# Performance work log

Measured on AMD Instinct MI355X. Metric: run time of the kernel, lower is better.

The kernel has to match this reference:

```python
import jax, jax.numpy as jnp
import numpy as np

NUM_EMBEDDINGS = 1024
EMBEDDING_DIM = 256
COMMITMENT_COST = 0.25
STRAIGHT_THROUGH = True


def setup_inputs() -> dict:
    key = jax.random.key(0)
    k_in, k_emb = jax.random.split(key)
    inputs = jax.random.normal(k_in, (32, 32, 32, EMBEDDING_DIM), dtype=jnp.float32)
    # variance_scaling(1.0, 'fan_in', 'uniform') over (K, D): limit = sqrt(3 / fan_in)
    limit = np.sqrt(3.0 / EMBEDDING_DIM).astype(np.float32)
    embedding = jax.random.uniform(
        k_emb, (NUM_EMBEDDINGS, EMBEDDING_DIM), dtype=jnp.float32,
        minval=-limit, maxval=limit)
    return {"inputs": inputs, "embedding": embedding}


def reference(inputs, embedding):
    input_shape = inputs.shape
    flat = jnp.reshape(inputs, (-1, EMBEDDING_DIM))  # [N, D]
    # squared euclidean distances [N, K]
    distances = (jnp.sum(flat ** 2, axis=1, keepdims=True)
                 - 2.0 * jnp.matmul(flat, embedding.T)
                 + jnp.sum(embedding ** 2, axis=1)[None, :])
    encoding_indices = jnp.argmin(distances, axis=1)  # [N]
    quantized = jnp.take(embedding, encoding_indices, axis=0)  # [N, D] gather == one-hot matmul
    quantized = jnp.reshape(quantized, input_shape)
    if STRAIGHT_THROUGH:
        quantized = inputs + jax.lax.stop_gradient(quantized - inputs)
    else:
        quantized = jax.lax.stop_gradient(quantized)
    e_latent_loss = jnp.mean((jax.lax.stop_gradient(quantized) - inputs) ** 2)
    q_latent_loss = jnp.mean((quantized - jax.lax.stop_gradient(inputs)) ** 2)
    vq_loss = q_latent_loss + COMMITMENT_COST * e_latent_loss
    return quantized, vq_loss, encoding_indices
```

## Files before the change

### kernel.cpp

```cpp
#include <hip/hip_runtime.h>

#define NPTS 32768
#define DIM 256
#define KCODES 1024
#define NSPLIT 8
#define BN 256
#define BKC 128
#define BK 64
#define MARGIN 0.08f

typedef __attribute__((ext_vector_type(8))) short short8v;
typedef __attribute__((ext_vector_type(8))) unsigned short ushort8v;
typedef __attribute__((ext_vector_type(4))) float f32x4;

static __device__ __forceinline__ unsigned short f2bf(float f) {
    unsigned int u = __float_as_uint(f);
    unsigned int r = (u + 0x7fffu + ((u >> 16) & 1u)) >> 16;
    return (unsigned short)r;
}

static __device__ __forceinline__ void gload16(const void* g, void* l) {
    __builtin_amdgcn_global_load_lds((const __attribute__((address_space(1))) void*)g,
                                     (__attribute__((address_space(3))) void*)l, 16, 0, 0);
}

__global__ void convert_kernel(const float* __restrict__ X, const float* __restrict__ E,
                               unsigned short* __restrict__ Xb, unsigned short* __restrict__ Eb) {
    int i = blockIdx.x * 256 + threadIdx.x;
    size_t e8 = (size_t)i * 8;
    const float* src; unsigned short* dst; size_t off;
    if (e8 < (size_t)NPTS * DIM) { src = X; dst = Xb; off = e8; }
    else { src = E; dst = Eb; off = e8 - (size_t)NPTS * DIM; }
    float4 f0 = *(const float4*)(src + off);
    float4 f1 = *(const float4*)(src + off + 4);
    ushort8v v;
    v[0] = f2bf(f0.x); v[1] = f2bf(f0.y); v[2] = f2bf(f0.z); v[3] = f2bf(f0.w);
    v[4] = f2bf(f1.x); v[5] = f2bf(f1.y); v[6] = f2bf(f1.z); v[7] = f2bf(f1.w);
    *(ushort8v*)(dst + off) = v;
}

__global__ void enormnp_kernel(const float* __restrict__ E, float* __restrict__ Cnp,
                               int* __restrict__ counter) {
#pragma clang fp contract(off)
    if (blockIdx.x == 0 && threadIdx.x == 0) counter[0] = 0;
    int k = blockIdx.x * 256 + threadIdx.x;
    const float* e = E + (size_t)k * DIM;
    float half[2];
    for (int h = 0; h < 2; ++h) {
        const float* b = e + h * 128;
        float s[8];
#pragma unroll
        for (int j = 0; j < 8; ++j) { float v = b[j]; s[j] = v * v; }
        for (int i = 8; i < 128; i += 8) {
#pragma unroll
            for (int j = 0; j < 8; ++j) { float v = b[i + j]; s[j] += v * v; }
        }
        half[h] = ((s[0] + s[1]) + (s[2] + s[3])) + ((s[4] + s[5]) + (s[6] + s[7]));
    }
    Cnp[k] = half[0] + half[1];
}

__global__ __launch_bounds__(256, 2) void dist_kernel(
        const unsigned short* __restrict__ Xb, const unsigned short* __restrict__ Eb,
        const float* __restrict__ Cnp,
        float* __restrict__ ws_mm, unsigned int* __restrict__ cand) {
    __shared__ unsigned short xs[BN * BK];
    __shared__ unsigned short es[BKC * BK];

    const int tid = threadIdx.x;
    const int lane = tid & 63;
    const int wave = tid >> 6;
    const int lg = lane >> 4, lc = lane & 15;
    const int pbase = blockIdx.x * BN;
    const int split = blockIdx.y;
    const int cbase = split * BKC;

    f32x4 acc[4][8];
#pragma unroll
    for (int i = 0; i < 4; ++i)
#pragma unroll
        for (int j = 0; j < 8; ++j) acc[i][j] = (f32x4){0.f, 0.f, 0.f, 0.f};

    for (int ks = 0; ks < DIM / BK; ++ks) {
        const int k0 = ks * BK;
        __syncthreads();
#pragma unroll
        for (int q = 0; q < 8; ++q) {
            const int B = wave * 8192 + q * 1024 + lane * 16;
            const int row = B >> 7;
            const int cs = ((B >> 4) & 7) ^ (row & 7);
            gload16(Xb + (size_t)(pbase + row) * DIM + k0 + cs * 8,
                    (char*)xs + wave * 8192 + q * 1024);
        }
#pragma unroll
        for (int q = 0; q < 4; ++q) {
            const int B = wave * 4096 + q * 1024 + lane * 16;
            const int row = B >> 7;
            const int cs = ((B >> 4) & 7) ^ (row & 7);
            gload16(Eb + (size_t)(cbase + row) * DIM + k0 + cs * 8,
                    (char*)es + wave * 4096 + q * 1024);
        }
        __syncthreads();
#pragma unroll
        for (int kk = 0; kk < 2; ++kk) {
            short8v a[4];
#pragma unroll
            for (int f = 0; f < 4; ++f) {
                int row = wave * 64 + f * 16 + lc;
                int cs = (kk * 4 + lg) ^ (row & 7);
                a[f] = *(const short8v*)&xs[row * BK + cs * 8];
            }
#pragma unroll
            for (int j = 0; j < 8; ++j) {
                int row = j * 16 + lc;
                int cs = (kk * 4 + lg) ^ (row & 7);
                short8v b = *(const short8v*)&es[row * BK + cs * 8];
#pragma unroll
                for (int i = 0; i < 4; ++i)
                    acc[i][j] = __builtin_amdgcn_mfma_f32_16x16x32_bf16(a[i], b, acc[i][j], 0, 0, 0);
            }
        }
    }

    float en8[8];
#pragma unroll
    for (int j = 0; j < 8; ++j) en8[j] = Cnp[cbase + j * 16 + lc];

    float m1[4][4], m2[4][4];
#pragma unroll
    for (int i = 0; i < 4; ++i)
#pragma unroll
        for (int r = 0; r < 4; ++r) { m1[i][r] = 3.4e38f; m2[i][r] = 3.4e38f; }

#pragma unroll
    for (int j = 0; j < 8; ++j)
#pragma unroll
        for (int i = 0; i < 4; ++i)
#pragma unroll
            for (int r = 0; r < 4; ++r) {
                float d = __builtin_fmaf(-2.f, acc[i][j][r], en8[j]);
                m2[i][r] = fminf(fmaxf(d, m1[i][r]), m2[i][r]);
                m1[i][r] = fminf(d, m1[i][r]);
            }

#pragma unroll
    for (int m = 1; m < 16; m <<= 1) {
#pragma unroll
        for (int i = 0; i < 4; ++i)
#pragma unroll
            for (int r = 0; r < 4; ++r) {
                float o1 = __shfl_xor(m1[i][r], m);
                float o2 = __shfl_xor(m2[i][r], m);
                float mx = fmaxf(m1[i][r], o1);
                m1[i][r] = fminf(m1[i][r], o1);
                m2[i][r] = fminf(fminf(m2[i][r], o2), mx);
            }
    }

#pragma unroll
    for (int i = 0; i < 4; ++i)
#pragma unroll
        for (int r = 0; r < 4; ++r) {
            float thr = m1[i][r] + MARGIN;
            unsigned int sl[8];
#pragma unroll
            for (int j = 0; j < 8; ++j) {
                float d = __builtin_fmaf(-2.f, acc[i][j][r], en8[j]);
                unsigned long long mm = __ballot(d <= thr);
                sl[j] = (unsigned int)((mm >> (lg * 16)) & 0xFFFFull);
            }
            if (lc == 0) {
                int p = pbase + wave * 64 + i * 16 + lg * 4 + r;
                uint4 w4 = { sl[0] | (sl[1] << 16), sl[2] | (sl[3] << 16),
                             sl[4] | (sl[5] << 16), sl[6] | (sl[7] << 16) };
                *(uint4*)&cand[((size_t)p * NSPLIT + split) * 4] = w4;
                float2 mm2 = { m1[i][r], m2[i][r] };
                *(float2*)&ws_mm[((size_t)p * NSPLIT + split) * 2] = mm2;
            }
        }
}

__global__ void resolve_kernel(const float* __restrict__ ws_mm, const unsigned int* __restrict__ cand,
                               int* __restrict__ final_idx, int* __restrict__ list,
                               int* __restrict__ counter) {
    const int p = blockIdx.x * 256 + threadIdx.x;
    float v1 = 3.4e38f, v2 = 3.4e38f;
    int sstar = 0;
#pragma unroll
    for (int s = 0; s < NSPLIT; ++s) {
        float2 mm = *(const float2*)&ws_mm[((size_t)p * NSPLIT + s) * 2];
        if (mm.x < v1) {
            v2 = fminf(v1, mm.y); v1 = mm.x; sstar = s;
        } else {
            v2 = fminf(v2, mm.x);
        }
    }
    uint4 w4 = *(const uint4*)&cand[((size_t)p * NSPLIT + sstar) * 4];
    int idx;
    if (w4.x)      idx = __builtin_ctz(w4.x);
    else if (w4.y) idx = 32 + __builtin_ctz(w4.y);
    else if (w4.z) idx = 64 + __builtin_ctz(w4.z);
    else           idx = 96 + __builtin_ctz(w4.w);
    final_idx[p] = sstar * BKC + idx;

    float thr = v1 + MARGIN;
    if (v2 <= thr) {
        int slot = atomicAdd(counter, 1);
        list[slot] = p;
    }
}

__global__ __launch_bounds__(256) void rescore_np_kernel(
        const float* __restrict__ X, const float* __restrict__ E,
        const float* __restrict__ Cnp, const unsigned int* __restrict__ cand,
        const int* __restrict__ list, const int* __restrict__ counter,
        int* __restrict__ final_idx) {
#pragma clang fp contract(off)
    const int tid = threadIdx.x;
    const int lane = tid & 63;
    const int wave = tid >> 6;
    const int cnt = counter[0];
    __shared__ float xsh[4][DIM];

    for (int base = blockIdx.x * 4; base < cnt; base += gridDim.x * 4) {
        const int li = base + wave;
        const bool active = (li < cnt);
        const int p = list[active ? li : (cnt - 1)];
        __syncthreads();
        *(float4*)&xsh[wave][lane * 4] = *(const float4*)(X + (size_t)p * DIM + lane * 4);
        __syncthreads();

        float s = 0.f;
        if (lane < 16) {
            const int h = lane >> 3, j = lane & 7;
            float v = xsh[wave][h * 128 + j];
            s = v * v;
            for (int i = 8; i < 128; i += 8) {
                float w = xsh[wave][h * 128 + i + j];
                s += w * w;
            }
        }
        float t0 = __shfl(s, 0), t1 = __shfl(s, 1), t2 = __shfl(s, 2), t3 = __shfl(s, 3);
        float t4 = __shfl(s, 4), t5 = __shfl(s, 5), t6 = __shfl(s, 6), t7 = __shfl(s, 7);
        float u0 = __shfl(s, 8), u1 = __shfl(s, 9), u2 = __shfl(s, 10), u3 = __shfl(s, 11);
        float u4 = __shfl(s, 12), u5 = __shfl(s, 13), u6 = __shfl(s, 14), u7 = __shfl(s, 15);
        const float A = (((t0 + t1) + (t2 + t3)) + ((t4 + t5) + (t6 + t7)))
                      + (((u0 + u1) + (u2 + u3)) + ((u4 + u5) + (u6 + u7)));

        float bv = 3.4e38f; int bi = 0x7FFFFFFF;
        if (lane < 32) {
            unsigned int bits = cand[(size_t)p * 32 + lane];
            const int cb = (lane >> 2) * 128 + (lane & 3) * 32;
            while (bits) {
                int t = __builtin_ctz(bits);
                bits &= bits - 1;
                int c = cb + t;
                const float4* er4 = (const float4*)(E + (size_t)c * DIM);
                float acc = 0.f;
                for (int d4 = 0; d4 < DIM / 4; ++d4) {
                    float4 e4 = er4[d4];
                    float4 x4 = *(const float4*)&xsh[wave][d4 * 4];
                    acc = __builtin_fmaf(x4.x, e4.x, acc);
                    acc = __builtin_fmaf(x4.y, e4.y, acc);
                    acc = __builtin_fmaf(x4.z, e4.z, acc);
                    acc = __builtin_fmaf(x4.w, e4.w, acc);
                }
                float tt = A - 2.0f * acc;
                float dnp = tt + Cnp[c];
                if (dnp < bv) { bv = dnp; bi = c; }
            }
        }
#pragma unroll
        for (int m = 1; m < 64; m <<= 1) {
            float ov = __shfl_xor(bv, m);
            int oi = __shfl_xor(bi, m);
            if (ov < bv || (ov == bv && oi < bi)) { bv = ov; bi = oi; }
        }
        if (active && lane == 0) final_idx[p] = bi;
    }
}

__global__ void gather_kernel(const float* __restrict__ X, const float* __restrict__ E,
                              const int* __restrict__ final_idx,
                              float* __restrict__ out_q, float* __restrict__ out_idx,
                              float* __restrict__ ws_part) {
    const int tid = threadIdx.x;
    const int p = blockIdx.x * 16 + (tid >> 4);
    const int c = tid & 15;
    const int bi = final_idx[p];

    float ls = 0.f;
#pragma unroll
    for (int k = 0; k < 4; ++k) {
        int d4 = c + k * 16;
        float4 e4 = *(const float4*)(E + (size_t)bi * DIM + d4 * 4);
        float4 x4 = *(const float4*)(X + (size_t)p * DIM + d4 * 4);
        *(float4*)(out_q + (size_t)p * DIM + d4 * 4) = e4;
        float dx = e4.x - x4.x, dy = e4.y - x4.y, dz = e4.z - x4.z, dw = e4.w - x4.w;
        ls += dx * dx + dy * dy + dz * dz + dw * dw;
    }
    if (c == 0) out_idx[p] = (float)bi;

    __shared__ float red[256];
    red[tid] = ls;
    __syncthreads();
#pragma unroll
    for (int s = 128; s > 0; s >>= 1) {
        if (tid < s) red[tid] += red[tid + s];
        __syncthreads();
    }
    if (tid == 0) ws_part[blockIdx.x] = red[0];
}

__global__ void loss_kernel(const float* __restrict__ ws_part, float* __restrict__ out_loss) {
    const int tid = threadIdx.x;
    float s = 0.f;
    for (int i = tid; i < NPTS / 16; i += 256) s += ws_part[i];
    __shared__ float red[256];
    red[tid] = s;
    __syncthreads();
#pragma unroll
    for (int t = 128; t > 0; t >>= 1) {
        if (tid < t) red[tid] += red[tid + t];
        __syncthreads();
    }
    if (tid == 0)
        out_loss[0] = (1.f + 0.25f) * red[0] / (float)((size_t)NPTS * DIM);
}

extern "C" void kernel_launch(void* const* d_in, const int* in_sizes, int n_in,
                              void* d_out, int out_size, void* d_ws, size_t ws_size,
                              hipStream_t stream) {
    const float* X = (const float*)d_in[0];
    const float* E = (const float*)d_in[1];
    float* out = (float*)d_out;
    float* out_q = out;
    float* out_loss = out + (size_t)NPTS * DIM;
    float* out_idx = out + (size_t)NPTS * DIM + 1;

    unsigned short* Xb = (unsigned short*)d_out;
    unsigned short* Eb = Xb + (size_t)NPTS * DIM;
    unsigned int* cand = (unsigned int*)(Eb + (size_t)KCODES * DIM);

    float* ws = (float*)d_ws;
    float* Cnp = ws;
    float* ws_mm = Cnp + KCODES;
    int* final_idx = (int*)(ws_mm + (size_t)NPTS * NSPLIT * 2);
    int* counter = final_idx + NPTS;
    int* list = counter + 64;
    float* ws_part = (float*)(list + NPTS);

    convert_kernel<<<(NPTS + KCODES) * DIM / 8 / 256, 256, 0, stream>>>(X, E, Xb, Eb);
    enormnp_kernel<<<KCODES / 256, 256, 0, stream>>>(E, Cnp, counter);
    dist_kernel<<<dim3(NPTS / BN, NSPLIT), 256, 0, stream>>>(Xb, Eb, Cnp, ws_mm, cand);
    resolve_kernel<<<NPTS / 256, 256, 0, stream>>>(ws_mm, cand, final_idx, list, counter);
    rescore_np_kernel<<<512, 256, 0, stream>>>(X, E, Cnp, cand, list, counter, final_idx);
    gather_kernel<<<NPTS / 16, 256, 0, stream>>>(X, E, final_idx, out_q, out_idx, ws_part);
    loss_kernel<<<1, 256, 0, stream>>>(ws_part, out_loss);
}
```

Measured before the change: 98.20 us.

## Fuse codebook norms into convert, compute loss from distances, drop second-min tracking

Folds the codebook-norm computation into the conversion kernel as extra blocks, and accumulates per-point ||x||^2 during conversion. The loss is then assembled from ||x||^2 plus the best bf16-approximate distance inside resolve via a last-block reduction, so gather no longer rereads X and the separate loss kernel is removed. Dist_kernel keeps only the running minimum, no second minimum, and raises launch bounds to 3 blocks per CU. Ambiguity is detected from the per-split minima and candidate popcount. Risks: the loss now uses approximate (bf16) distances that are not rescored, and register pressure rises under the tighter occupancy target.

```diff
diff --git a/kernel.cpp b/kernel.cpp
--- a/kernel.cpp
+++ b/kernel.cpp
@@ -8,6 +8,7 @@
 #define BKC 128
 #define BK 64
 #define MARGIN 0.08f
+#define CVT_BLOCKS 2048
 
 typedef __attribute__((ext_vector_type(8))) short short8v;
 typedef __attribute__((ext_vector_type(8))) unsigned short ushort8v;
@@ -25,45 +26,62 @@
 }
 
 __global__ void convert_kernel(const float* __restrict__ X, const float* __restrict__ E,
-                               unsigned short* __restrict__ Xb, unsigned short* __restrict__ Eb) {
-    int i = blockIdx.x * 256 + threadIdx.x;
-    size_t e8 = (size_t)i * 8;
-    const float* src; unsigned short* dst; size_t off;
-    if (e8 < (size_t)NPTS * DIM) { src = X; dst = Xb; off = e8; }
-    else { src = E; dst = Eb; off = e8 - (size_t)NPTS * DIM; }
-    float4 f0 = *(const float4*)(src + off);
-    float4 f1 = *(const float4*)(src + off + 4);
-    ushort8v v;
-    v[0] = f2bf(f0.x); v[1] = f2bf(f0.y); v[2] = f2bf(f0.z); v[3] = f2bf(f0.w);
-    v[4] = f2bf(f1.x); v[5] = f2bf(f1.y); v[6] = f2bf(f1.z); v[7] = f2bf(f1.w);
-    *(ushort8v*)(dst + off) = v;
-}
-
-__global__ void enormnp_kernel(const float* __restrict__ E, float* __restrict__ Cnp,
-                               int* __restrict__ counter) {
+                               unsigned short* __restrict__ Xb, unsigned short* __restrict__ Eb,
+                               float* __restrict__ Cnp, float* __restrict__ xsq_part) {
 #pragma clang fp contract(off)
-    if (blockIdx.x == 0 && threadIdx.x == 0) counter[0] = 0;
-    int k = blockIdx.x * 256 + threadIdx.x;
-    const float* e = E + (size_t)k * DIM;
-    float half[2];
-    for (int h = 0; h < 2; ++h) {
-        const float* b = e + h * 128;
-        float s[8];
-#pragma unroll
-        for (int j = 0; j < 8; ++j) { float v = b[j]; s[j] = v * v; }
-        for (int i = 8; i < 128; i += 8) {
-#pragma unroll
-            for (int j = 0; j < 8; ++j) { float v = b[i + j]; s[j] += v * v; }
-        }
-        half[h] = ((s[0] + s[1]) + (s[2] + s[3])) + ((s[4] + s[5]) + (s[6] + s[7]));
-    }
-    Cnp[k] = half[0] + half[1];
-}
-
-__global__ __launch_bounds__(256, 2) void dist_kernel(
+    const int tid = threadIdx.x;
+    if (blockIdx.x >= CVT_BLOCKS) {
+        int k = (blockIdx.x - CVT_BLOCKS) * 256 + tid;
+        const float* e = E + (size_t)k * DIM;
+        float half[2];
+        for (int h = 0; h < 2; ++h) {
+            const float* b = e + h * 128;
+            float s[8];
+#pragma unroll
+            for (int j = 0; j < 8; ++j) { float v = b[j]; s[j] = v * v; }
+            for (int i = 8; i < 128; i += 8) {
+#pragma unroll
+                for (int j = 0; j < 8; ++j) { float v = b[i + j]; s[j] += v * v; }
+            }
+            half[h] = ((s[0] + s[1]) + (s[2] + s[3])) + ((s[4] + s[5]) + (s[6] + s[7]));
+        }
+        Cnp[k] = half[0] + half[1];
+        return;
+    }
+    const int total = (NPTS + KCODES) * DIM / 8;
+    float xsq = 0.f;
+    for (int i = blockIdx.x * 256 + tid; i < total; i += CVT_BLOCKS * 256) {
+        size_t e8 = (size_t)i * 8;
+        const float* src; unsigned short* dst; size_t off;
+        bool isX = e8 < (size_t)NPTS * DIM;
+        if (isX) { src = X; dst = Xb; off = e8; }
+        else { src = E; dst = Eb; off = e8 - (size_t)NPTS * DIM; }
+        float4 f0 = *(const float4*)(src + off);
+        float4 f1 = *(const float4*)(src + off + 4);
+        ushort8v v;
+        v[0] = f2bf(f0.x); v[1] = f2bf(f0.y); v[2] = f2bf(f0.z); v[3] = f2bf(f0.w);
+        v[4] = f2bf(f1.x); v[5] = f2bf(f1.y); v[6] = f2bf(f1.z); v[7] = f2bf(f1.w);
+        *(ushort8v*)(dst + off) = v;
+        if (isX)
+            xsq += f0.x * f0.x + f0.y * f0.y + f0.z * f0.z + f0.w * f0.w
+                 + f1.x * f1.x + f1.y * f1.y + f1.z * f1.z + f1.w * f1.w;
+    }
+    __shared__ float red[256];
+    red[tid] = xsq;
+    __syncthreads();
+#pragma unroll
+    for (int s = 128; s > 0; s >>= 1) {
+        if (tid < s) red[tid] += red[tid + s];
+        __syncthreads();
+    }
+    if (tid == 0) xsq_part[blockIdx.x] = red[0];
+}
+
+__global__ __launch_bounds__(256, 3) void dist_kernel(
         const unsigned short* __restrict__ Xb, const unsigned short* __restrict__ Eb,
         const float* __restrict__ Cnp,
-        float* __restrict__ ws_mm, unsigned int* __restrict__ cand) {
+        float* __restrict__ ws_m1, unsigned int* __restrict__ cand,
+        int* __restrict__ counters) {
     __shared__ unsigned short xs[BN * BK];
     __shared__ unsigned short es[BKC * BK];
 
@@ -75,6 +93,8 @@
     const int split = blockIdx.y;
     const int cbase = split * BKC;
 
+    if (blockIdx.x == 0 && split == 0 && tid == 0) { counters[0] = 0; counters[32] = 0; }
+
     f32x4 acc[4][8];
 #pragma unroll
     for (int i = 0; i < 4; ++i)
@@ -126,36 +146,25 @@
 #pragma unroll
     for (int j = 0; j < 8; ++j) en8[j] = Cnp[cbase + j * 16 + lc];
 
-    float m1[4][4], m2[4][4];
+    float m1[4][4];
 #pragma unroll
     for (int i = 0; i < 4; ++i)
 #pragma unroll
-        for (int r = 0; r < 4; ++r) { m1[i][r] = 3.4e38f; m2[i][r] = 3.4e38f; }
-
+        for (int r = 0; r < 4; ++r) m1[i][r] = 3.4e38f;
 #pragma unroll
     for (int j = 0; j < 8; ++j)
 #pragma unroll
         for (int i = 0; i < 4; ++i)
 #pragma unroll
-            for (int r = 0; r < 4; ++r) {
-                float d = __builtin_fmaf(-2.f, acc[i][j][r], en8[j]);
-                m2[i][r] = fminf(fmaxf(d, m1[i][r]), m2[i][r]);
-                m1[i][r] = fminf(d, m1[i][r]);
-            }
-
-#pragma unroll
-    for (int m = 1; m < 16; m <<= 1) {
+            for (int r = 0; r < 4; ++r)
+                m1[i][r] = fminf(m1[i][r], __builtin_fmaf(-2.f, acc[i][j][r], en8[j]));
+#pragma unroll
+    for (int m = 1; m < 16; m <<= 1)
 #pragma unroll
         for (int i = 0; i < 4; ++i)
 #pragma unroll
-            for (int r = 0; r < 4; ++r) {
-                float o1 = __shfl_xor(m1[i][r], m);
-                float o2 = __shfl_xor(m2[i][r], m);
-                float mx = fmaxf(m1[i][r], o1);
-                m1[i][r] = fminf(m1[i][r], o1);
-                m2[i][r] = fminf(fminf(m2[i][r], o2), mx);
-            }
-    }
+            for (int r = 0; r < 4; ++r)
+                m1[i][r] = fminf(m1[i][r], __shfl_xor(m1[i][r], m));
 
 #pragma unroll
     for (int i = 0; i < 4; ++i)
@@ -174,52 +183,89 @@
                 uint4 w4 = { sl[0] | (sl[1] << 16), sl[2] | (sl[3] << 16),
                              sl[4] | (sl[5] << 16), sl[6] | (sl[7] << 16) };
                 *(uint4*)&cand[((size_t)p * NSPLIT + split) * 4] = w4;
-                float2 mm2 = { m1[i][r], m2[i][r] };
-                *(float2*)&ws_mm[((size_t)p * NSPLIT + split) * 2] = mm2;
-            }
-        }
-}
-
-__global__ void resolve_kernel(const float* __restrict__ ws_mm, const unsigned int* __restrict__ cand,
+                ws_m1[(size_t)p * NSPLIT + split] = m1[i][r];
+            }
+        }
+}
+
+__global__ void resolve_kernel(const float* __restrict__ ws_m1, const unsigned int* __restrict__ cand,
                                int* __restrict__ final_idx, int* __restrict__ list,
-                               int* __restrict__ counter) {
-    const int p = blockIdx.x * 256 + threadIdx.x;
-    float v1 = 3.4e38f, v2 = 3.4e38f;
-    int sstar = 0;
-#pragma unroll
-    for (int s = 0; s < NSPLIT; ++s) {
-        float2 mm = *(const float2*)&ws_mm[((size_t)p * NSPLIT + s) * 2];
-        if (mm.x < v1) {
-            v2 = fminf(v1, mm.y); v1 = mm.x; sstar = s;
-        } else {
-            v2 = fminf(v2, mm.x);
-        }
-    }
+                               int* __restrict__ counters,
+                               const float* __restrict__ xsq_part, float* __restrict__ v1_part,
+                               float* __restrict__ out_loss) {
+    const int tid = threadIdx.x;
+    const int p = blockIdx.x * 256 + tid;
+    float4 ma = *(const float4*)&ws_m1[(size_t)p * NSPLIT];
+    float4 mb = *(const float4*)&ws_m1[(size_t)p * NSPLIT + 4];
+    float m[8] = { ma.x, ma.y, ma.z, ma.w, mb.x, mb.y, mb.z, mb.w };
+    float v1 = m[0]; int sstar = 0;
+#pragma unroll
+    for (int s = 1; s < NSPLIT; ++s)
+        if (m[s] < v1) { v1 = m[s]; sstar = s; }
+    float thr = v1 + MARGIN;
+    bool flag = false;
+#pragma unroll
+    for (int s = 0; s < NSPLIT; ++s)
+        if (s != sstar && m[s] <= thr) flag = true;
     uint4 w4 = *(const uint4*)&cand[((size_t)p * NSPLIT + sstar) * 4];
+    int pc = __builtin_popcount(w4.x) + __builtin_popcount(w4.y)
+           + __builtin_popcount(w4.z) + __builtin_popcount(w4.w);
+    flag = flag || (pc > 1);
     int idx;
     if (w4.x)      idx = __builtin_ctz(w4.x);
     else if (w4.y) idx = 32 + __builtin_ctz(w4.y);
     else if (w4.z) idx = 64 + __builtin_ctz(w4.z);
     else           idx = 96 + __builtin_ctz(w4.w);
     final_idx[p] = sstar * BKC + idx;
-
-    float thr = v1 + MARGIN;
-    if (v2 <= thr) {
-        int slot = atomicAdd(counter, 1);
+    if (flag) {
+        int slot = atomicAdd(&counters[0], 1);
         list[slot] = p;
+    }
+
+    __shared__ float red[256];
+    red[tid] = v1;
+    __syncthreads();
+#pragma unroll
+    for (int s = 128; s > 0; s >>= 1) {
+        if (tid < s) red[tid] += red[tid + s];
+        __syncthreads();
+    }
+    if (tid == 0) v1_part[blockIdx.x] = red[0];
+
+    __shared__ int amlast;
+    if (tid == 0) {
+        __threadfence();
+        amlast = (atomicAdd(&counters[32], 1) == (int)gridDim.x - 1);
+    }
+    __syncthreads();
+    if (amlast) {
+        __threadfence();
+        double s = 0.0;
+        for (int i = tid; i < CVT_BLOCKS; i += 256) s += (double)xsq_part[i];
+        for (int i = tid; i < NPTS / 256; i += 256) s += (double)v1_part[i];
+        __shared__ double dred[256];
+        dred[tid] = s;
+        __syncthreads();
+#pragma unroll
+        for (int t = 128; t > 0; t >>= 1) {
+            if (tid < t) dred[tid] += dred[tid + t];
+            __syncthreads();
+        }
+        if (tid == 0)
+            out_loss[0] = (float)(1.25 * dred[0] / (double)((size_t)NPTS * DIM));
     }
 }
 
 __global__ __launch_bounds__(256) void rescore_np_kernel(
         const float* __restrict__ X, const float* __restrict__ E,
         const float* __restrict__ Cnp, const unsigned int* __restrict__ cand,
-        const int* __restrict__ list, const int* __restrict__ counter,
+        const int* __restrict__ list, const int* __restrict__ counters,
         int* __restrict__ final_idx) {
 #pragma clang fp contract(off)
     const int tid = threadIdx.x;
     const int lane = tid & 63;
     const int wave = tid >> 6;
-    const int cnt = counter[0];
+    const int cnt = counters[0];
     __shared__ float xsh[4][DIM];
 
     for (int base = blockIdx.x * 4; base < cnt; base += gridDim.x * 4) {
@@ -280,52 +326,19 @@
     }
 }
 
-__global__ void gather_kernel(const float* __restrict__ X, const float* __restrict__ E,
-                              const int* __restrict__ final_idx,
-                              float* __restrict__ out_q, float* __restrict__ out_idx,
-                              float* __restrict__ ws_part) {
+__global__ void gather_kernel(const float* __restrict__ E, const int* __restrict__ final_idx,
+                              float* __restrict__ out_q, float* __restrict__ out_idx) {
     const int tid = threadIdx.x;
     const int p = blockIdx.x * 16 + (tid >> 4);
     const int c = tid & 15;
     const int bi = final_idx[p];
-
-    float ls = 0.f;
 #pragma unroll
     for (int k = 0; k < 4; ++k) {
         int d4 = c + k * 16;
         float4 e4 = *(const float4*)(E + (size_t)bi * DIM + d4 * 4);
-        float4 x4 = *(const float4*)(X + (size_t)p * DIM + d4 * 4);
         *(float4*)(out_q + (size_t)p * DIM + d4 * 4) = e4;
-        float dx = e4.x - x4.x, dy = e4.y - x4.y, dz = e4.z - x4.z, dw = e4.w - x4.w;
-        ls += dx * dx + dy * dy + dz * dz + dw * dw;
     }
     if (c == 0) out_idx[p] = (float)bi;
-
-    __shared__ float red[256];
-    red[tid] = ls;
-    __syncthreads();
-#pragma unroll
-    for (int s = 128; s > 0; s >>= 1) {
-        if (tid < s) red[tid] += red[tid + s];
-        __syncthreads();
-    }
-    if (tid == 0) ws_part[blockIdx.x] = red[0];
-}
-
-__global__ void loss_kernel(const float* __restrict__ ws_part, float* __restrict__ out_loss) {
-    const int tid = threadIdx.x;
-    float s = 0.f;
-    for (int i = tid; i < NPTS / 16; i += 256) s += ws_part[i];
-    __shared__ float red[256];
-    red[tid] = s;
-    __syncthreads();
-#pragma unroll
-    for (int t = 128; t > 0; t >>= 1) {
-        if (tid < t) red[tid] += red[tid + t];
-        __syncthreads();
-    }
-    if (tid == 0)
-        out_loss[0] = (1.f + 0.25f) * red[0] / (float)((size_t)NPTS * DIM);
 }
 
 extern "C" void kernel_launch(void* const* d_in, const int* in_sizes, int n_in,
@@ -344,17 +357,17 @@
 
     float* ws = (float*)d_ws;
     float* Cnp = ws;
-    float* ws_mm = Cnp + KCODES;
-    int* final_idx = (int*)(ws_mm + (size_t)NPTS * NSPLIT * 2);
-    int* counter = final_idx + NPTS;
-    int* list = counter + 64;
-    float* ws_part = (float*)(list + NPTS);
-
-    convert_kernel<<<(NPTS + KCODES) * DIM / 8 / 256, 256, 0, stream>>>(X, E, Xb, Eb);
-    enormnp_kernel<<<KCODES / 256, 256, 0, stream>>>(E, Cnp, counter);
-    dist_kernel<<<dim3(NPTS / BN, NSPLIT), 256, 0, stream>>>(Xb, Eb, Cnp, ws_mm, cand);
-    resolve_kernel<<<NPTS / 256, 256, 0, stream>>>(ws_mm, cand, final_idx, list, counter);
-    rescore_np_kernel<<<512, 256, 0, stream>>>(X, E, Cnp, cand, list, counter, final_idx);
-    gather_kernel<<<NPTS / 16, 256, 0, stream>>>(X, E, final_idx, out_q, out_idx, ws_part);
-    loss_kernel<<<1, 256, 0, stream>>>(ws_part, out_loss);
-}
+    float* ws_m1 = Cnp + KCODES;
+    int* final_idx = (int*)(ws_m1 + (size_t)NPTS * NSPLIT);
+    int* counters = final_idx + NPTS;
+    int* list = counters + 64;
+    float* xsq_part = (float*)(list + NPTS);
+    float* v1_part = xsq_part + CVT_BLOCKS;
+
+    convert_kernel<<<CVT_BLOCKS + KCODES / 256, 256, 0, stream>>>(X, E, Xb, Eb, Cnp, xsq_part);
+    dist_kernel<<<dim3(NPTS / BN, NSPLIT), 256, 0, stream>>>(Xb, Eb, Cnp, ws_m1, cand, counters);
+    resolve_kernel<<<NPTS / 256, 256, 0, stream>>>(ws_m1, cand, final_idx, list, counters,
+                                                   xsq_part, v1_part, out_loss);
+    rescore_np_kernel<<<512, 256, 0, stream>>>(X, E, Cnp, cand, list, counters, final_idx);
+    gather_kernel<<<NPTS / 16, 256, 0, stream>>>(E, final_idx, out_q, out_idx);
+}
```

After: 119.8 us. 22.0% more time.
